# Kernel optimization log

Hardware: AMD Instinct MI355X
Metric: run time of the kernel (lower is better)

Reference implementation:

```python
import jax, jax.numpy as jnp
import numpy as np

HEAD_SIZE = 64

def setup_inputs() -> dict:
    key = jax.random.key(0)
    ks = jax.random.split(key, 7)
    B, S, H, D = 8, 2048, 768, HEAD_SIZE
    scale = 1.0 / np.sqrt(H)
    return {
        "x": jax.random.normal(ks[0], (B, S, H), dtype=jnp.float32),
        "Wq": jax.random.normal(ks[1], (H, D), dtype=jnp.float32) * scale,
        "bq": jax.random.normal(ks[2], (D,), dtype=jnp.float32) * 0.02,
        "Wk": jax.random.normal(ks[3], (H, D), dtype=jnp.float32) * scale,
        "bk": jax.random.normal(ks[4], (D,), dtype=jnp.float32) * 0.02,
        "Wv": jax.random.normal(ks[5], (H, D), dtype=jnp.float32) * scale,
        "bv": jax.random.normal(ks[6], (D,), dtype=jnp.float32) * 0.02,
    }

def reference(x, Wq, bq, Wk, bk, Wv, bv):
    # Q/K/V projections: [B,S,H] @ [H,D] -> [B,S,D]
    q = x @ Wq + bq
    k = x @ Wk + bk
    v = x @ Wv + bv
    # scaled dot-product scores: [B,S,S]
    scores = jnp.einsum("bsd,btd->bst", q, k) / jnp.sqrt(jnp.float32(HEAD_SIZE))
    probs = jax.nn.softmax(scores, axis=-1)
    # dropout p=0.0 -> identity (matches eval / p=0 training)
    out = jnp.einsum("bst,btd->bsd", probs, v)
    return (out, probs)
```

## Files before the change

kernel.cpp:

```cpp
#include <hip/hip_runtime.h>

#define BB 8
#define SS 2048
#define HH 768
#define DD 64
#define BK 64
#define NK (HH / BK)

typedef short bf16x8 __attribute__((ext_vector_type(8)));
typedef short bf16x4 __attribute__((ext_vector_type(4)));
typedef float f32x16 __attribute__((ext_vector_type(16)));
typedef float f32x4 __attribute__((ext_vector_type(4)));

#define EXPC 0.18033688011112042f

static __device__ __forceinline__ short f2bf(float f) {
    union { float f; unsigned u; } v; v.f = f;
    unsigned u = v.u + 0x7fff + ((v.u >> 16) & 1);
    return (short)(u >> 16);
}

static __device__ __forceinline__ int sigma(int j) {
    return (j & 19) | ((j & 4) << 1) | ((j & 8) >> 1);
}

__global__ __launch_bounds__(256) void w_convert(
    const float* __restrict__ Wq, const float* __restrict__ Wk,
    const float* __restrict__ Wv, short* __restrict__ wT)
{
    __shared__ float ws[64][65];
    const int jj   = blockIdx.x / 12;
    const int h0   = (blockIdx.x % 12) * 64;
    const int tid  = threadIdx.x;
    const float* Wsrc = (jj == 0) ? Wq : (jj == 1 ? Wk : Wv);

    {
        const int hl = tid >> 4;
        const int c4 = tid & 15;
        #pragma unroll
        for (int p = 0; p < 4; ++p) {
            const int h = hl + p * 16;
            float4 v = ((const float4*)(Wsrc + (long)(h0 + h) * DD))[c4];
            ws[h][c4 * 4 + 0] = v.x; ws[h][c4 * 4 + 1] = v.y;
            ws[h][c4 * 4 + 2] = v.z; ws[h][c4 * 4 + 3] = v.w;
        }
    }
    __syncthreads();

    const int d   = tid >> 2;
    const int seg = tid & 3;
    bf16x8 t0, t1;
    #pragma unroll
    for (int m = 0; m < 8; ++m) {
        t0[m] = f2bf(ws[seg * 16 + m][d]);
        t1[m] = f2bf(ws[seg * 16 + 8 + m][d]);
    }
    short* dst = wT + ((long)jj * 64 + d) * HH + h0 + seg * 16;
    *(bf16x8*)dst = t0;
    *(bf16x8*)(dst + 8) = t1;
}

__global__ __launch_bounds__(384) void qkv_mfma(
    const float* __restrict__ x, const short* __restrict__ wT,
    const float* __restrict__ bq, const float* __restrict__ bk,
    const float* __restrict__ bv,
    short* __restrict__ qo, short* __restrict__ ko, short* __restrict__ vT)
{
    __shared__ short xs[2][32][68];

    const int tid  = threadIdx.x;
    const int w    = tid >> 6;
    const int lane = tid & 63;
    const int l31  = lane & 31;
    const int h    = lane >> 5;
    const long row0 = (long)blockIdx.x * 32;

    const int r0 = tid >> 4,        c0 = tid & 15;
    const int r1 = (tid + 384) >> 4, c1 = (tid + 384) & 15;
    const bool has1 = (tid + 384) < 512;

    f32x16 acc;
    #pragma unroll
    for (int i = 0; i < 16; ++i) acc[i] = 0.f;

    float4 st0, st1;
    st0 = ((const float4*)(x + (row0 + r0) * HH))[c0];
    if (has1) st1 = ((const float4*)(x + (row0 + r1) * HH))[c1];
    {
        bf16x4 b0; b0[0]=f2bf(st0.x); b0[1]=f2bf(st0.y); b0[2]=f2bf(st0.z); b0[3]=f2bf(st0.w);
        *(bf16x4*)&xs[0][r0][c0 * 4] = b0;
        if (has1) {
            bf16x4 b1; b1[0]=f2bf(st1.x); b1[1]=f2bf(st1.y); b1[2]=f2bf(st1.z); b1[3]=f2bf(st1.w);
            *(bf16x4*)&xs[0][r1][c1 * 4] = b1;
        }
    }
    __syncthreads();

    const int col = w * 32 + l31;
    const short* wcol = wT + (long)col * HH + h * 8;

    for (int it = 0; it < NK; ++it) {
        const int cur = it & 1;
        if (it < NK - 1) {
            st0 = ((const float4*)(x + (row0 + r0) * HH + (it + 1) * BK))[c0];
            if (has1) st1 = ((const float4*)(x + (row0 + r1) * HH + (it + 1) * BK))[c1];
        }
        #pragma unroll
        for (int kt = 0; kt < 4; ++kt) {
            bf16x8 af = *(const bf16x8*)&xs[cur][l31][kt * 16 + h * 8];
            bf16x8 bf = *(const bf16x8*)(wcol + it * BK + kt * 16);
            acc = __builtin_amdgcn_mfma_f32_32x32x16_bf16(af, bf, acc, 0, 0, 0);
        }
        if (it < NK - 1) {
            __syncthreads();
            bf16x4 b0; b0[0]=f2bf(st0.x); b0[1]=f2bf(st0.y); b0[2]=f2bf(st0.z); b0[3]=f2bf(st0.w);
            *(bf16x4*)&xs[cur ^ 1][r0][c0 * 4] = b0;
            if (has1) {
                bf16x4 b1; b1[0]=f2bf(st1.x); b1[1]=f2bf(st1.y); b1[2]=f2bf(st1.z); b1[3]=f2bf(st1.w);
                *(bf16x4*)&xs[cur ^ 1][r1][c1 * 4] = b1;
            }
            __syncthreads();
        }
    }

    short (*vs)[68] = xs[0];
    const int j = w >> 1;
    const int d = (w & 1) * 32 + l31;
    const float* bptr = (j == 0) ? bq : (j == 1 ? bk : bv);
    const float bias = bptr[d];

    __syncthreads();

    #pragma unroll
    for (int i = 0; i < 16; ++i) {
        const int r = (i & 3) + 8 * (i >> 2) + 4 * h;
        const short val = f2bf(acc[i] + bias);
        if (j == 0)      qo[(row0 + r) * DD + d] = val;
        else if (j == 1) ko[(row0 + r) * DD + d] = val;
        else             vs[r][d] = val;
    }
    __syncthreads();

    if (tid < 256) {
        const int b  = (int)(row0 >> 11);
        const int s0 = (int)(row0 & (SS - 1));
        const int dd  = tid >> 2;
        const int seg = tid & 3;
        bf16x8 t;
        #pragma unroll
        for (int m = 0; m < 8; ++m) t[m] = vs[seg * 8 + m][dd];
        *(bf16x8*)(vT + ((long)b * DD + dd) * SS + s0 + seg * 8) = t;
    }
}

__global__ __launch_bounds__(512) void attn(
    const short* __restrict__ qb, const short* __restrict__ kb,
    const short* __restrict__ vT,
    float* __restrict__ out, float* __restrict__ probs)
{
    __shared__ float obuf[32][65];
    __shared__ float sumbuf[32][9];

    const int tid  = threadIdx.x;
    const int w    = tid >> 6;
    const int lane = tid & 63;
    const int l31  = lane & 31;
    const int h    = lane >> 5;

    const int b    = blockIdx.x & 7;
    const int row0 = (blockIdx.x >> 3) * 32;
    const int wk0  = w * 256;

    for (int i = tid; i < 32 * 65; i += 512) ((float*)obuf)[i] = 0.f;

    bf16x8 qf[4];
    const short* qrow = qb + ((long)(b * SS) + row0 + l31) * DD + h * 8;
    #pragma unroll
    for (int kt = 0; kt < 4; ++kt) qf[kt] = *(const bf16x8*)(qrow + kt * 16);

    const int sl = sigma(l31);
    const short* kbase = kb + ((long)(b * SS) + wk0 + sl) * DD + h * 8;
    const short* vbase = vT + (long)b * DD * SS + wk0 + h * 8;

    unsigned P8[8][8];
    f32x16 oacc[2];
    #pragma unroll
    for (int i = 0; i < 16; ++i) { oacc[0][i] = 0.f; oacc[1][i] = 0.f; }
    float s = 0.f;

    #pragma unroll
    for (int ct = 0; ct < 8; ++ct) {
        const short* kp = kbase + (long)ct * 32 * DD;
        f32x16 a;
        #pragma unroll
        for (int i = 0; i < 16; ++i) a[i] = 0.f;
        #pragma unroll
        for (int kt = 0; kt < 4; ++kt) {
            bf16x8 kf = *(const bf16x8*)(kp + kt * 16);
            a = __builtin_amdgcn_mfma_f32_32x32x16_bf16(kf, qf[kt], a, 0, 0, 0);
        }
        #pragma unroll
        for (int i = 0; i < 16; ++i) {
            a[i] = __builtin_amdgcn_exp2f(a[i] * EXPC);
            s += a[i];
        }
        #pragma unroll
        for (int i = 0; i < 8; ++i) {
            unsigned u;
            asm("v_cvt_pk_bf16_f32 %0, %1, %2"
                : "=v"(u) : "v"(a[2 * i]), "v"(a[2 * i + 1]));
            P8[ct][i] = u;
        }
        #pragma unroll
        for (int kk = 0; kk < 2; ++kk) {
            union { unsigned u[4]; bf16x8 v; } pf;
            pf.u[0] = P8[ct][4 * kk + 0]; pf.u[1] = P8[ct][4 * kk + 1];
            pf.u[2] = P8[ct][4 * kk + 2]; pf.u[3] = P8[ct][4 * kk + 3];
            #pragma unroll
            for (int nt = 0; nt < 2; ++nt) {
                bf16x8 vf = *(const bf16x8*)(vbase + (long)(nt * 32 + l31) * SS
                                             + ct * 32 + kk * 16);
                oacc[nt] = __builtin_amdgcn_mfma_f32_32x32x16_bf16(vf, pf.v, oacc[nt], 0, 0, 0);
            }
        }
    }

    s += __shfl_xor(s, 32);
    if (lane < 32) sumbuf[l31][w] = s;
    __syncthreads();
    float gs = 0.f;
    #pragma unroll
    for (int i = 0; i < 8; ++i) gs += sumbuf[l31][i];
    const float inv = 1.f / gs;

    float* prow = probs + ((long)(b * SS) + row0 + l31) * SS + wk0 + 8 * h;
    #pragma unroll
    for (int ct = 0; ct < 8; ++ct) {
        f32x4 o0, o1, o2, o3;
        #pragma unroll
        for (int i = 0; i < 2; ++i) {
            const unsigned u0 = P8[ct][2 * i + 0], u1 = P8[ct][2 * i + 1];
            o0[2 * i + 0] = __uint_as_float(u0 << 16) * inv;
            o0[2 * i + 1] = __uint_as_float(u0 & 0xffff0000u) * inv;
            o1[2 * i + 0] = __uint_as_float(u1 << 16) * inv;
            o1[2 * i + 1] = __uint_as_float(u1 & 0xffff0000u) * inv;
        }
        #pragma unroll
        for (int i = 0; i < 2; ++i) {
            const unsigned u0 = P8[ct][4 + 2 * i], u1 = P8[ct][5 + 2 * i];
            o2[2 * i + 0] = __uint_as_float(u0 << 16) * inv;
            o2[2 * i + 1] = __uint_as_float(u0 & 0xffff0000u) * inv;
            o3[2 * i + 0] = __uint_as_float(u1 << 16) * inv;
            o3[2 * i + 1] = __uint_as_float(u1 & 0xffff0000u) * inv;
        }
        float* pp = prow + ct * 32;
        f32x4 q0, q1, q2, q3;
        q0[0] = __uint_as_float(P8[ct][0] << 16) * inv;
        q0[1] = __uint_as_float(P8[ct][0] & 0xffff0000u) * inv;
        q0[2] = __uint_as_float(P8[ct][1] << 16) * inv;
        q0[3] = __uint_as_float(P8[ct][1] & 0xffff0000u) * inv;
        q1[0] = __uint_as_float(P8[ct][2] << 16) * inv;
        q1[1] = __uint_as_float(P8[ct][2] & 0xffff0000u) * inv;
        q1[2] = __uint_as_float(P8[ct][3] << 16) * inv;
        q1[3] = __uint_as_float(P8[ct][3] & 0xffff0000u) * inv;
        q2[0] = __uint_as_float(P8[ct][4] << 16) * inv;
        q2[1] = __uint_as_float(P8[ct][4] & 0xffff0000u) * inv;
        q2[2] = __uint_as_float(P8[ct][5] << 16) * inv;
        q2[3] = __uint_as_float(P8[ct][5] & 0xffff0000u) * inv;
        q3[0] = __uint_as_float(P8[ct][6] << 16) * inv;
        q3[1] = __uint_as_float(P8[ct][6] & 0xffff0000u) * inv;
        q3[2] = __uint_as_float(P8[ct][7] << 16) * inv;
        q3[3] = __uint_as_float(P8[ct][7] & 0xffff0000u) * inv;
        *(f32x4*)(pp)          = q0;
        *(f32x4*)(pp + 4)      = q1;
        *(f32x4*)(pp + 16)     = q2;
        *(f32x4*)(pp + 16 + 4) = q3;
    }

    #pragma unroll
    for (int nt = 0; nt < 2; ++nt)
        #pragma unroll
        for (int i = 0; i < 16; ++i)
            atomicAdd(&obuf[l31][nt * 32 + (i & 3) + 8 * (i >> 2) + 4 * h],
                      oacc[nt][i] * inv);
    __syncthreads();

    {
        const int q   = tid >> 4;
        const int seg = tid & 15;
        float4 val = make_float4(obuf[q][seg * 4 + 0], obuf[q][seg * 4 + 1],
                                 obuf[q][seg * 4 + 2], obuf[q][seg * 4 + 3]);
        *(float4*)(out + ((long)(b * SS) + row0 + q) * DD + seg * 4) = val;
    }
}

extern "C" void kernel_launch(void* const* d_in, const int* in_sizes, int n_in,
                              void* d_out, int out_size, void* d_ws, size_t ws_size,
                              hipStream_t stream) {
    const float* x  = (const float*)d_in[0];
    const float* Wq = (const float*)d_in[1];
    const float* bq = (const float*)d_in[2];
    const float* Wk = (const float*)d_in[3];
    const float* bk = (const float*)d_in[4];
    const float* Wv = (const float*)d_in[5];
    const float* bv = (const float*)d_in[6];

    float* out   = (float*)d_out;
    float* probs = (float*)d_out + (long)BB * SS * DD;

    short* q  = (short*)d_ws;
    short* k  = q + (long)BB * SS * DD;
    short* vT = k + (long)BB * SS * DD;
    short* wT = vT + (long)BB * SS * DD;

    w_convert<<<36, 256, 0, stream>>>(Wq, Wk, Wv, wT);
    qkv_mfma<<<(BB * SS) / 32, 384, 0, stream>>>(x, wT, bq, bk, bv, q, k, vT);
    attn<<<BB * (SS / 32), 512, 0, stream>>>(q, k, vT, out, probs);
}
```

Before: 123.7 us.

## Stage probs through LDS for coalesced nontemporal stores and raise MFMA priority

The probs output is now staged through a per-wave LDS tile, so that each group of 8 lanes writes one contiguous 128-byte row segment with nontemporal float4 stores. Before, each lane wrote scattered 16-byte pieces. The change also raises wave priority with s_setprio around the MFMA/exp loop to favour compute issue. It aims to speed up the dominant 537 MB probs write, at the cost of about 35 KB of extra LDS, which may lower occupancy.

Result: faster. 120.9 us (-2.3%).

```diff
diff --git a/kernel.cpp b/kernel.cpp
--- a/kernel.cpp
+++ b/kernel.cpp
@@ -158,6 +158,7 @@
     const short* __restrict__ vT,
     float* __restrict__ out, float* __restrict__ probs)
 {
+    __shared__ float pbuf[8][32][34];
     __shared__ float obuf[32][65];
     __shared__ float sumbuf[32][9];
 
@@ -194,6 +195,7 @@
         f32x16 a;
         #pragma unroll
         for (int i = 0; i < 16; ++i) a[i] = 0.f;
+        __builtin_amdgcn_s_setprio(1);
         #pragma unroll
         for (int kt = 0; kt < 4; ++kt) {
             bf16x8 kf = *(const bf16x8*)(kp + kt * 16);
@@ -223,6 +225,7 @@
                 oacc[nt] = __builtin_amdgcn_mfma_f32_32x32x16_bf16(vf, pf.v, oacc[nt], 0, 0, 0);
             }
         }
+        __builtin_amdgcn_s_setprio(0);
     }
 
     s += __shfl_xor(s, 32);
@@ -233,48 +236,30 @@
     for (int i = 0; i < 8; ++i) gs += sumbuf[l31][i];
     const float inv = 1.f / gs;
 
-    float* prow = probs + ((long)(b * SS) + row0 + l31) * SS + wk0 + 8 * h;
+    const int qq  = lane >> 3, sg2 = lane & 7;
+    float* prow_base = probs + ((long)(b * SS) + row0) * SS + wk0;
+
     #pragma unroll
     for (int ct = 0; ct < 8; ++ct) {
-        f32x4 o0, o1, o2, o3;
-        #pragma unroll
-        for (int i = 0; i < 2; ++i) {
-            const unsigned u0 = P8[ct][2 * i + 0], u1 = P8[ct][2 * i + 1];
-            o0[2 * i + 0] = __uint_as_float(u0 << 16) * inv;
-            o0[2 * i + 1] = __uint_as_float(u0 & 0xffff0000u) * inv;
-            o1[2 * i + 0] = __uint_as_float(u1 << 16) * inv;
-            o1[2 * i + 1] = __uint_as_float(u1 & 0xffff0000u) * inv;
-        }
-        #pragma unroll
-        for (int i = 0; i < 2; ++i) {
-            const unsigned u0 = P8[ct][4 + 2 * i], u1 = P8[ct][5 + 2 * i];
-            o2[2 * i + 0] = __uint_as_float(u0 << 16) * inv;
-            o2[2 * i + 1] = __uint_as_float(u0 & 0xffff0000u) * inv;
-            o3[2 * i + 0] = __uint_as_float(u1 << 16) * inv;
-            o3[2 * i + 1] = __uint_as_float(u1 & 0xffff0000u) * inv;
-        }
-        float* pp = prow + ct * 32;
-        f32x4 q0, q1, q2, q3;
-        q0[0] = __uint_as_float(P8[ct][0] << 16) * inv;
-        q0[1] = __uint_as_float(P8[ct][0] & 0xffff0000u) * inv;
-        q0[2] = __uint_as_float(P8[ct][1] << 16) * inv;
-        q0[3] = __uint_as_float(P8[ct][1] & 0xffff0000u) * inv;
-        q1[0] = __uint_as_float(P8[ct][2] << 16) * inv;
-        q1[1] = __uint_as_float(P8[ct][2] & 0xffff0000u) * inv;
-        q1[2] = __uint_as_float(P8[ct][3] << 16) * inv;
-        q1[3] = __uint_as_float(P8[ct][3] & 0xffff0000u) * inv;
-        q2[0] = __uint_as_float(P8[ct][4] << 16) * inv;
-        q2[1] = __uint_as_float(P8[ct][4] & 0xffff0000u) * inv;
-        q2[2] = __uint_as_float(P8[ct][5] << 16) * inv;
-        q2[3] = __uint_as_float(P8[ct][5] & 0xffff0000u) * inv;
-        q3[0] = __uint_as_float(P8[ct][6] << 16) * inv;
-        q3[1] = __uint_as_float(P8[ct][6] & 0xffff0000u) * inv;
-        q3[2] = __uint_as_float(P8[ct][7] << 16) * inv;
-        q3[3] = __uint_as_float(P8[ct][7] & 0xffff0000u) * inv;
-        *(f32x4*)(pp)          = q0;
-        *(f32x4*)(pp + 4)      = q1;
-        *(f32x4*)(pp + 16)     = q2;
-        *(f32x4*)(pp + 16 + 4) = q3;
+        #pragma unroll
+        for (int i = 0; i < 8; ++i) {
+            const unsigned u = P8[ct][i];
+            float2 f2;
+            f2.x = __uint_as_float(u << 16) * inv;
+            f2.y = __uint_as_float(u & 0xffff0000u) * inv;
+            const int colp = 16 * (i >> 2) + 8 * h + ((2 * i) & 7);
+            *(float2*)&pbuf[w][l31][colp] = f2;
+        }
+        #pragma unroll
+        for (int jj = 0; jj < 4; ++jj) {
+            const int q = qq + 8 * jj;
+            float2 a2 = *(float2*)&pbuf[w][q][sg2 * 4];
+            float2 b2 = *(float2*)&pbuf[w][q][sg2 * 4 + 2];
+            f32x4 o4;
+            o4[0] = a2.x; o4[1] = a2.y; o4[2] = b2.x; o4[3] = b2.y;
+            __builtin_nontemporal_store(o4,
+                (f32x4*)(prow_base + (long)q * SS + ct * 32 + sg2 * 4));
+        }
     }
 
     #pragma unroll
```
